# Kernel tuning notes

Hardware: AMD Instinct MI355X
Metric: run time of the kernel (lower is better)

## Reference

```python
import jax, jax.numpy as jnp
import numpy as np

B, L, DH = 8, 4096, 1024
T, DG, P = 1024, 768, 256
EPS = 1e-8


def setup_inputs() -> dict:
    key = jax.random.key(0)
    k1, k2, k3, k4 = jax.random.split(key, 4)
    H = jax.random.normal(k1, (B, L, DH), dtype=jnp.float32)
    G = jax.random.normal(k2, (B, T, DG), dtype=jnp.float32)
    # nn.Linear(d, P, bias=False) weights: shape [P, d], uniform(-1/sqrt(d), 1/sqrt(d))
    Wq = jax.random.uniform(k3, (P, DG), jnp.float32, -1.0, 1.0) / jnp.sqrt(jnp.float32(DG))
    Wk = jax.random.uniform(k4, (P, DH), jnp.float32, -1.0, 1.0) / jnp.sqrt(jnp.float32(DH))
    return {"H": H, "G": G, "Wq": Wq, "Wk": Wk}


def reference(H, G, Wq, Wk):
    # Chunked online-softmax streaming is mathematically equivalent to one
    # full stable softmax cross-attention pass; values are the raw H.
    scale = jnp.float32(P) ** -0.5
    Q = jnp.einsum("btd,pd->btp", G, Wq)          # [B,T,P]
    K = jnp.einsum("bld,pd->blp", H, Wk)          # [B,L,P]
    logits = jnp.einsum("btp,blp->btl", Q, K).astype(jnp.float32) * scale
    m = jnp.max(logits, axis=-1, keepdims=True)
    p = jnp.exp(logits - m)                        # [B,T,L]
    s = jnp.sum(p, axis=-1, keepdims=True)         # [B,T,1]
    z = jnp.einsum("btl,bld->btd", p, H.astype(jnp.float32))
    Z = (z / (s + EPS)).astype(H.dtype)            # [B,T,DH]
    return Z
```

## Files before the change

kernel.cpp:

```cpp
#include <hip/hip_runtime.h>
#include <hip/hip_bf16.h>
#include <stdint.h>

#define Bn  8
#define Ln  4096
#define DHn 1024
#define Tn  1024
#define DGn 768
#define Pn  256

typedef float  f32x4  __attribute__((ext_vector_type(4)));
typedef __bf16 bf16x8 __attribute__((ext_vector_type(8)));

__device__ __forceinline__ void gload16(const void* g, void* l) {
  __builtin_amdgcn_global_load_lds(
      (const __attribute__((address_space(1))) void*)g,
      (__attribute__((address_space(3))) void*)l, 16, 0, 0);
}

__device__ __forceinline__ unsigned short f2bf(float x) {
  union { float f; uint32_t u; } v; v.f = x;
  uint32_t u = v.u;
  return (unsigned short)((u + 0x7FFFu + ((u >> 16) & 1u)) >> 16);
}

__device__ __forceinline__ float bf2f(unsigned short b) {
  union { uint32_t u; float f; } v; v.u = ((uint32_t)b) << 16;
  return v.f;
}

__global__ void cvt_kernel(const float4* __restrict__ in,
                           ushort4* __restrict__ out, int n4) {
  int i = blockIdx.x * 256 + threadIdx.x;
  if (i < n4) {
    float4 v = in[i];
    ushort4 o;
    o.x = f2bf(v.x); o.y = f2bf(v.y); o.z = f2bf(v.z); o.w = f2bf(v.w);
    out[i] = o;
  }
}

__global__ void prep_H(const float* __restrict__ Hg,
                       unsigned short* __restrict__ Hb,
                       unsigned short* __restrict__ HT) {
  __shared__ unsigned short tile[64 * 65];
  const int b  = blockIdx.z;
  const int l0 = blockIdx.x * 64;
  const int d0 = blockIdx.y * 64;
  const float4* src  = (const float4*)(Hg + (size_t)b * Ln * DHn);
  ushort4*      dstH = (ushort4*)(Hb + (size_t)b * Ln * DHn);
  for (int e = threadIdx.x; e < 1024; e += 256) {
    int l  = e >> 4;
    int d4 = e & 15;
    size_t idx4 = ((size_t)(l0 + l) * DHn + d0) / 4 + d4;
    float4 v = src[idx4];
    ushort4 o;
    o.x = f2bf(v.x); o.y = f2bf(v.y); o.z = f2bf(v.z); o.w = f2bf(v.w);
    dstH[idx4] = o;
    int d = d4 * 4;
    tile[(d + 0) * 65 + l] = o.x;
    tile[(d + 1) * 65 + l] = o.y;
    tile[(d + 2) * 65 + l] = o.z;
    tile[(d + 3) * 65 + l] = o.w;
  }
  __syncthreads();
  ushort4* dst = (ushort4*)(HT + (size_t)b * DHn * Ln);
  for (int e = threadIdx.x; e < 1024; e += 256) {
    int d  = e >> 4;
    int l4 = (e & 15) * 4;
    ushort4 o;
    o.x = tile[d * 65 + l4 + 0];
    o.y = tile[d * 65 + l4 + 1];
    o.z = tile[d * 65 + l4 + 2];
    o.w = tile[d * 65 + l4 + 3];
    dst[((size_t)(d0 + d) * Ln + l0) / 4 + (e & 15)] = o;
  }
}

template <int EPI, int NT, int BK>
__global__ __launch_bounds__(256) void gemm_bt(
    const unsigned short* __restrict__ A, const unsigned short* __restrict__ B,
    void* __restrict__ Cout, float* __restrict__ S,
    int kLen, int lda, int ldb, int ldc,
    long sA, long sB, long sC, int sS, float scale, int nTiles) {
  constexpr int Nn  = NT * 32;
  constexpr int RPC = 1024 / (BK * 2);
  constexpr int APW = (128 * BK * 2 / 1024) / 4;
  constexpr int BPW = (Nn  * BK * 2 / 1024) / 4;
  __shared__ unsigned short As[128 * BK];
  __shared__ unsigned short Bs[Nn * BK];
  int x = blockIdx.x;
  const int b = x & (Bn - 1);
  int r = x >> 3;
  const int ni = r % nTiles;
  const int mi = r / nTiles;
  const unsigned short* Ab = A + (long)b * sA;
  const unsigned short* Bb = B + (long)b * sB;
  const int m0 = mi * 128;
  const int n0 = ni * Nn;
  const int tid  = threadIdx.x;
  const int lane = tid & 63;
  const int wave = tid >> 6;
  const int wm = (wave >> 1) << 6;
  const int wn = (wave & 1) * (NT * 16);
  const int lrow = lane & 15;
  const int quad = lane >> 4;
  const int srow  = (BK == 32) ? (lane >> 2) : (lane >> 3);
  const int skcol = (BK == 32)
      ? (((lane & 3) ^ ((lane >> 3) & 3)) << 3)
      : (((lane & 7) ^ ((lane >> 3) & 7)) << 3);

  f32x4 acc[4][NT];
#pragma unroll
  for (int mt = 0; mt < 4; ++mt)
#pragma unroll
    for (int nt = 0; nt < NT; ++nt) acc[mt][nt] = f32x4{0.f, 0.f, 0.f, 0.f};

  for (int k0 = 0; k0 < kLen; k0 += BK) {
    __syncthreads();
#pragma unroll
    for (int j = 0; j < APW; ++j) {
      int c = wave * APW + j;
      gload16(Ab + (size_t)(m0 + c * RPC + srow) * lda + (k0 + skcol), &As[c * 512]);
    }
#pragma unroll
    for (int j = 0; j < BPW; ++j) {
      int c = wave * BPW + j;
      gload16(Bb + (size_t)(n0 + c * RPC + srow) * ldb + (k0 + skcol), &Bs[c * 512]);
    }
    __syncthreads();
#pragma unroll
    for (int h = 0; h < BK / 32; ++h) {
      const int fsl = (BK == 32)
          ? ((quad ^ ((lrow >> 1) & 3)) << 3)
          : ((((h << 2) + quad) ^ (lrow & 7)) << 3);
      bf16x8 af[4], bfr[NT];
#pragma unroll
      for (int mt = 0; mt < 4; ++mt)
        af[mt] = *(const bf16x8*)&As[(wm + mt * 16 + lrow) * BK + fsl];
#pragma unroll
      for (int nt = 0; nt < NT; ++nt)
        bfr[nt] = *(const bf16x8*)&Bs[(wn + nt * 16 + lrow) * BK + fsl];
#pragma unroll
      for (int mt = 0; mt < 4; ++mt)
#pragma unroll
        for (int nt = 0; nt < NT; ++nt)
          acc[mt][nt] = __builtin_amdgcn_mfma_f32_16x16x32_bf16(
              af[mt], bfr[nt], acc[mt][nt], 0, 0, 0);
    }
  }

  if (EPI == 0) {
    unsigned short* C = (unsigned short*)Cout + (long)b * sC;
#pragma unroll
    for (int mt = 0; mt < 4; ++mt)
#pragma unroll
      for (int r2 = 0; r2 < 4; ++r2) {
        int row = m0 + wm + mt * 16 + quad * 4 + r2;
        unsigned short* Cr = C + (size_t)row * ldc + n0 + wn + lrow;
#pragma unroll
        for (int nt = 0; nt < NT; ++nt) Cr[nt * 16] = f2bf(acc[mt][nt][r2]);
      }
  } else if (EPI == 1) {
    unsigned short* C = (unsigned short*)Cout + (long)b * sC;
    float* Sb = S + (long)b * sS;
#pragma unroll
    for (int mt = 0; mt < 4; ++mt)
#pragma unroll
      for (int r2 = 0; r2 < 4; ++r2) {
        int row = m0 + wm + mt * 16 + quad * 4 + r2;
        unsigned short* Cr = C + (size_t)row * ldc + n0 + wn + lrow;
        float psum = 0.f;
#pragma unroll
        for (int nt = 0; nt < NT; ++nt) {
          float e = __expf(acc[mt][nt][r2] * scale);
          unsigned short bv = f2bf(e);
          Cr[nt * 16] = bv;
          psum += bf2f(bv);
        }
        psum += __shfl_xor(psum, 1);
        psum += __shfl_xor(psum, 2);
        psum += __shfl_xor(psum, 4);
        psum += __shfl_xor(psum, 8);
        if (lrow == 0) atomicAdd(&Sb[row], psum);
      }
  } else {
    float* C = (float*)Cout + (long)b * sC;
    const float* Sb = S + (long)b * sS;
#pragma unroll
    for (int mt = 0; mt < 4; ++mt)
#pragma unroll
      for (int r2 = 0; r2 < 4; ++r2) {
        int row = m0 + wm + mt * 16 + quad * 4 + r2;
        float inv = 1.f / (Sb[row] + 1e-8f);
        float* Cr = C + (size_t)row * ldc + n0 + wn + lrow;
#pragma unroll
        for (int nt = 0; nt < NT; ++nt) Cr[nt * 16] = acc[mt][nt][r2] * inv;
      }
  }
}

extern "C" void kernel_launch(void* const* d_in, const int* in_sizes, int n_in,
                              void* d_out, int out_size, void* d_ws, size_t ws_size,
                              hipStream_t stream) {
  const float* H  = (const float*)d_in[0];
  const float* G  = (const float*)d_in[1];
  const float* Wq = (const float*)d_in[2];
  const float* Wk = (const float*)d_in[3];
  float* out = (float*)d_out;

  char* ws = (char*)d_ws;
  size_t off = 0;
  auto alloc = [&](size_t bytes) {
    void* p = ws + off;
    off = (off + bytes + 255) & ~(size_t)255;
    return p;
  };
  unsigned short* Hb  = (unsigned short*)alloc((size_t)Bn * Ln * DHn * 2);
  unsigned short* HbT = (unsigned short*)alloc((size_t)Bn * DHn * Ln * 2);
  unsigned short* Gb  = (unsigned short*)alloc((size_t)Bn * Tn * DGn * 2);
  unsigned short* Wqb = (unsigned short*)alloc((size_t)Pn * DGn * 2);
  unsigned short* Wkb = (unsigned short*)alloc((size_t)Pn * DHn * 2);
  unsigned short* Kb  = (unsigned short*)alloc((size_t)Bn * Ln * Pn * 2);
  unsigned short* Qb  = (unsigned short*)alloc((size_t)Bn * Tn * Pn * 2);
  float* Sv           = (float*)alloc((size_t)Bn * Tn * 4);
  unsigned short* Pm = Hb;

  {
    int n4 = Bn * Tn * DGn / 4;
    cvt_kernel<<<(n4 + 255) / 256, 256, 0, stream>>>((const float4*)G, (ushort4*)Gb, n4);
  }
  {
    int n4 = Pn * DGn / 4;
    cvt_kernel<<<(n4 + 255) / 256, 256, 0, stream>>>((const float4*)Wq, (ushort4*)Wqb, n4);
  }
  {
    int n4 = Pn * DHn / 4;
    cvt_kernel<<<(n4 + 255) / 256, 256, 0, stream>>>((const float4*)Wk, (ushort4*)Wkb, n4);
  }
  prep_H<<<dim3(Ln / 64, DHn / 64, Bn), 256, 0, stream>>>(H, Hb, HbT);
  hipMemsetAsync(Sv, 0, (size_t)Bn * Tn * 4, stream);

  gemm_bt<0, 2, 64><<<Bn * 32 * 4, 256, 0, stream>>>(
      Hb, Wkb, Kb, nullptr, DHn, DHn, DHn, Pn,
      (long)Ln * DHn, 0L, (long)Ln * Pn, 0, 1.f, 4);
  gemm_bt<0, 2, 64><<<Bn * 8 * 4, 256, 0, stream>>>(
      Gb, Wqb, Qb, nullptr, DGn, DGn, DGn, Pn,
      (long)Tn * DGn, 0L, (long)Tn * Pn, 0, 1.f, 4);
  gemm_bt<1, 4, 32><<<Bn * 8 * 32, 256, 0, stream>>>(
      Qb, Kb, Pm, Sv, Pn, Pn, Pn, Ln,
      (long)Tn * Pn, (long)Ln * Pn, (long)Tn * Ln, Tn, 0.0625f, 32);
  gemm_bt<2, 2, 64><<<Bn * 8 * 16, 256, 0, stream>>>(
      Pm, HbT, out, Sv, Ln, Ln, Ln, DHn,
      (long)Tn * Ln, (long)DHn * Ln, (long)Tn * DHn, Tn, 1.f, 16);
}
```

Before: 429.5 us.

## Double-buffer LDS in P·V GEMM and widen its N tile

After: 501.0 us. 16.7% more time.

```diff
diff --git a/kernel.cpp b/kernel.cpp
--- a/kernel.cpp
+++ b/kernel.cpp
@@ -77,7 +77,7 @@
   }
 }
 
-template <int EPI, int NT, int BK>
+template <int EPI, int NT, int BK, int DB>
 __global__ __launch_bounds__(256) void gemm_bt(
     const unsigned short* __restrict__ A, const unsigned short* __restrict__ B,
     void* __restrict__ Cout, float* __restrict__ S,
@@ -87,8 +87,9 @@
   constexpr int RPC = 1024 / (BK * 2);
   constexpr int APW = (128 * BK * 2 / 1024) / 4;
   constexpr int BPW = (Nn  * BK * 2 / 1024) / 4;
-  __shared__ unsigned short As[128 * BK];
-  __shared__ unsigned short Bs[Nn * BK];
+  constexpr int NB  = DB ? 2 : 1;
+  __shared__ unsigned short As[NB * 128 * BK];
+  __shared__ unsigned short Bs[NB * Nn * BK];
   int x = blockIdx.x;
   const int b = x & (Bn - 1);
   int r = x >> 3;
@@ -116,19 +117,24 @@
 #pragma unroll
     for (int nt = 0; nt < NT; ++nt) acc[mt][nt] = f32x4{0.f, 0.f, 0.f, 0.f};
 
-  for (int k0 = 0; k0 < kLen; k0 += BK) {
-    __syncthreads();
+  auto stage = [&](int k0, int buf) {
 #pragma unroll
     for (int j = 0; j < APW; ++j) {
       int c = wave * APW + j;
-      gload16(Ab + (size_t)(m0 + c * RPC + srow) * lda + (k0 + skcol), &As[c * 512]);
+      gload16(Ab + (size_t)(m0 + c * RPC + srow) * lda + (k0 + skcol),
+              &As[buf * (128 * BK) + c * 512]);
     }
 #pragma unroll
     for (int j = 0; j < BPW; ++j) {
       int c = wave * BPW + j;
-      gload16(Bb + (size_t)(n0 + c * RPC + srow) * ldb + (k0 + skcol), &Bs[c * 512]);
-    }
-    __syncthreads();
+      gload16(Bb + (size_t)(n0 + c * RPC + srow) * ldb + (k0 + skcol),
+              &Bs[buf * (Nn * BK) + c * 512]);
+    }
+  };
+
+  auto compute = [&](int buf) {
+    const int ab = buf * (128 * BK);
+    const int bb = buf * (Nn * BK);
 #pragma unroll
     for (int h = 0; h < BK / 32; ++h) {
       const int fsl = (BK == 32)
@@ -137,16 +143,41 @@
       bf16x8 af[4], bfr[NT];
 #pragma unroll
       for (int mt = 0; mt < 4; ++mt)
-        af[mt] = *(const bf16x8*)&As[(wm + mt * 16 + lrow) * BK + fsl];
+        af[mt] = *(const bf16x8*)&As[ab + (wm + mt * 16 + lrow) * BK + fsl];
 #pragma unroll
       for (int nt = 0; nt < NT; ++nt)
-        bfr[nt] = *(const bf16x8*)&Bs[(wn + nt * 16 + lrow) * BK + fsl];
+        bfr[nt] = *(const bf16x8*)&Bs[bb + (wn + nt * 16 + lrow) * BK + fsl];
 #pragma unroll
       for (int mt = 0; mt < 4; ++mt)
 #pragma unroll
         for (int nt = 0; nt < NT; ++nt)
           acc[mt][nt] = __builtin_amdgcn_mfma_f32_16x16x32_bf16(
               af[mt], bfr[nt], acc[mt][nt], 0, 0, 0);
+    }
+  };
+
+  if constexpr (DB) {
+    stage(0, 0);
+    __syncthreads();
+    int k0 = 0;
+    while (true) {
+      if (k0 + BK < kLen) stage(k0 + BK, 1);
+      compute(0);
+      __syncthreads();
+      k0 += BK;
+      if (k0 >= kLen) break;
+      if (k0 + BK < kLen) stage(k0 + BK, 0);
+      compute(1);
+      __syncthreads();
+      k0 += BK;
+      if (k0 >= kLen) break;
+    }
+  } else {
+    for (int k0 = 0; k0 < kLen; k0 += BK) {
+      __syncthreads();
+      stage(k0, 0);
+      __syncthreads();
+      compute(0);
     }
   }
 
@@ -241,16 +272,16 @@
   prep_H<<<dim3(Ln / 64, DHn / 64, Bn), 256, 0, stream>>>(H, Hb, HbT);
   hipMemsetAsync(Sv, 0, (size_t)Bn * Tn * 4, stream);
 
-  gemm_bt<0, 2, 64><<<Bn * 32 * 4, 256, 0, stream>>>(
+  gemm_bt<0, 2, 64, 0><<<Bn * 32 * 4, 256, 0, stream>>>(
       Hb, Wkb, Kb, nullptr, DHn, DHn, DHn, Pn,
       (long)Ln * DHn, 0L, (long)Ln * Pn, 0, 1.f, 4);
-  gemm_bt<0, 2, 64><<<Bn * 8 * 4, 256, 0, stream>>>(
+  gemm_bt<0, 2, 64, 0><<<Bn * 8 * 4, 256, 0, stream>>>(
       Gb, Wqb, Qb, nullptr, DGn, DGn, DGn, Pn,
       (long)Tn * DGn, 0L, (long)Tn * Pn, 0, 1.f, 4);
-  gemm_bt<1, 4, 32><<<Bn * 8 * 32, 256, 0, stream>>>(
+  gemm_bt<1, 4, 32, 0><<<Bn * 8 * 32, 256, 0, stream>>>(
       Qb, Kb, Pm, Sv, Pn, Pn, Pn, Ln,
       (long)Tn * Pn, (long)Ln * Pn, (long)Tn * Ln, Tn, 0.0625f, 32);
-  gemm_bt<2, 2, 64><<<Bn * 8 * 16, 256, 0, stream>>>(
+  gemm_bt<2, 4, 64, 1><<<Bn * 8 * 8, 256, 0, stream>>>(
       Pm, HbT, out, Sv, Ln, Ln, Ln, DHn,
-      (long)Tn * Ln, (long)DHn * Ln, (long)Tn * DHn, Tn, 1.f, 16);
-}
+      (long)Tn * Ln, (long)DHn * Ln, (long)Tn * DHn, Tn, 1.f, 8);
+}
```
